# Kernel optimization log

Measured on AMD Instinct MI355X. Metric: run time of the kernel, lower is better.

Reference implementation:

```python
import jax, jax.numpy as jnp
import numpy as np

N_NODES = 50000
N_EDGES = 500000
IN_DIM = 256
HEADS = 4
OUT_C = 64
NEG_SLOPE = 0.2


def setup_inputs() -> dict:
    key = jax.random.key(0)
    ks = jax.random.split(key, 6)
    x = jax.random.normal(ks[0], (N_NODES, IN_DIM), dtype=jnp.float32)
    edge_index = jax.random.randint(ks[1], (2, N_EDGES), 0, N_NODES, dtype=jnp.int64)
    scale = 1.0 / np.sqrt(IN_DIM)
    W_l = jax.random.normal(ks[2], (IN_DIM, HEADS * OUT_C), dtype=jnp.float32) * scale
    W_r = jax.random.normal(ks[3], (IN_DIM, HEADS * OUT_C), dtype=jnp.float32) * scale
    b_l = jnp.zeros((HEADS * OUT_C,), dtype=jnp.float32)
    b_r = jnp.zeros((HEADS * OUT_C,), dtype=jnp.float32)
    att = jax.random.normal(ks[4], (HEADS, OUT_C), dtype=jnp.float32) * (1.0 / np.sqrt(OUT_C))
    bias = jnp.zeros((HEADS * OUT_C,), dtype=jnp.float32)
    return {"x": x, "edge_index": edge_index, "W_l": W_l, "b_l": b_l,
            "W_r": W_r, "b_r": b_r, "att": att, "bias": bias}


def _gatv2(x, edge_index, W_l, b_l, W_r, b_r, att, bias):
    N = x.shape[0]
    H, C = att.shape
    # add self loops (PyG GATv2Conv default add_self_loops=True)
    loop = jnp.arange(N, dtype=edge_index.dtype)
    src = jnp.concatenate([edge_index[0], loop])  # message sources (x_j)
    dst = jnp.concatenate([edge_index[1], loop])  # aggregation targets (x_i)
    x_l = (x @ W_l + b_l).reshape(N, H, C)  # source-side projection
    x_r = (x @ W_r + b_r).reshape(N, H, C)  # target-side projection
    # GATv2 attention logits: a^T LeakyReLU(x_l[src] + x_r[dst])
    e = jax.nn.leaky_relu(x_l[src] + x_r[dst], NEG_SLOPE)  # [E, H, C]
    logits = jnp.einsum('ehc,hc->eh', e, att)              # [E, H]
    # segmented softmax over incoming edges of each dst node
    m = jax.ops.segment_max(logits, dst, num_segments=N)   # [N, H]
    ex = jnp.exp(logits - m[dst])
    denom = jax.ops.segment_sum(ex, dst, num_segments=N)   # [N, H]
    alpha = ex / denom[dst]                                # [E, H]
    # weighted scatter-aggregation of source messages
    out = jax.ops.segment_sum(x_l[src] * alpha[:, :, None], dst, num_segments=N)  # [N, H, C]
    return out.reshape(N, H * C) + bias


def reference(x, edge_index, W_l, b_l, W_r, b_r, att, bias):
    out = _gatv2(x, edge_index, W_l, b_l, W_r, b_r, att, bias)  # [N, H*C]
    # wrapper: single relation -> reshape(-1, 1, output_dim) and cat on dim=1
    return out.reshape(-1, 1, HEADS * OUT_C)
```

## Files before the change

### kernel.cpp

```cpp
#include <hip/hip_runtime.h>
#include <hip/hip_bf16.h>
#include <math.h>

#define N_NODES 50000
#define N_PAD   50048
#define N_EDGES 500000
#define E_TOT   550000
#define HC      256
#define NHC     512
#define HEADS   4
#define NEG     0.2f

typedef __attribute__((ext_vector_type(8))) short short8;
typedef __attribute__((ext_vector_type(4))) float f32x4;
typedef __attribute__((ext_vector_type(2))) float f32x2;

__device__ __forceinline__ ushort f2bf(float f) {
    union { float f; unsigned u; } c; c.f = f;
    unsigned u = c.u;
    unsigned rounded = u + 0x7FFFu + ((u >> 16) & 1u);
    return (ushort)(rounded >> 16);
}

static constexpr size_t OFF_COUNTS = 0;
static constexpr size_t OFF_CUR    = OFF_COUNTS + (size_t)N_NODES * 4;
static constexpr size_t OFF_ROWS   = OFF_CUR + (size_t)N_NODES * 4;
static constexpr size_t OFF_SRCS   = OFF_ROWS + (size_t)(N_NODES + 1) * 4;
static constexpr size_t OFF_BSUM   = OFF_SRCS + (size_t)E_TOT * 4;
static constexpr size_t OFF_MODE   = OFF_BSUM + 64 * 4;
static constexpr size_t OFF_XB     = ((OFF_MODE + 4 + 255) / 256) * 256;
static constexpr size_t OFF_WT     = OFF_XB + (size_t)N_PAD * HC * 2;
static constexpr size_t OFF_XLB    = OFF_WT + (size_t)NHC * HC * 2;
static constexpr size_t OFF_XRB    = OFF_XLB + (size_t)N_NODES * HC * 2;

__device__ __forceinline__ int get_src(const int* __restrict__ ei, int mode, int e) {
    if (e >= N_EDGES) return e - N_EDGES;
    return mode ? ei[2 * e] : ei[e];
}
__device__ __forceinline__ int get_dst(const int* __restrict__ ei, int mode, int e) {
    if (e >= N_EDGES) return e - N_EDGES;
    return mode ? ei[2 * (N_EDGES + e)] : ei[N_EDGES + e];
}

#define XBLK 6256
#define WBLK 512
__global__ __launch_bounds__(256) void prep_kernel(
        const float* __restrict__ x, const float* __restrict__ Wl,
        const float* __restrict__ Wr, const int* __restrict__ ei,
        ushort* __restrict__ xb, ushort* __restrict__ wt, int* __restrict__ mode) {
    const int b = blockIdx.x;
    if (b < XBLK) {
        size_t i = ((size_t)b * 256 + threadIdx.x) * 8;
        if (i >= (size_t)N_PAD * HC) return;
        ushort o[8];
        if (i < (size_t)N_NODES * HC) {
            float4 v0 = *(const float4*)(x + i);
            float4 v1 = *(const float4*)(x + i + 4);
            o[0] = f2bf(v0.x); o[1] = f2bf(v0.y); o[2] = f2bf(v0.z); o[3] = f2bf(v0.w);
            o[4] = f2bf(v1.x); o[5] = f2bf(v1.y); o[6] = f2bf(v1.z); o[7] = f2bf(v1.w);
        } else {
#pragma unroll
            for (int j = 0; j < 8; ++j) o[j] = 0;
        }
        *(short8*)(xb + i) = *(short8*)o;
    } else if (b < XBLK + WBLK) {
        int i = (b - XBLK) * 256 + threadIdx.x;
        int n = i >> 8, k = i & 255;
        float v = (n < HC) ? Wl[(size_t)k * HC + n] : Wr[(size_t)k * HC + (n - HC)];
        wt[i] = f2bf(v);
    } else {
        __shared__ int any;
        if (threadIdx.x == 0) any = 0;
        __syncthreads();
        if (ei[2 * threadIdx.x + 1] != 0) atomicOr(&any, 1);
        __syncthreads();
        if (threadIdx.x == 0) mode[0] = (any == 0) ? 1 : 0;
    }
}

#define BM 128
#define BK 32
__global__ __launch_bounds__(256) void mfma_gemm_kernel(
        const __hip_bfloat16* __restrict__ xb, const __hip_bfloat16* __restrict__ wt,
        const float* __restrict__ bl, const float* __restrict__ br,
        ushort* __restrict__ xlb, ushort* __restrict__ xrb) {
    __shared__ __hip_bfloat16 As[2][BM * BK];
    __shared__ __hip_bfloat16 Bs[2][BM * BK];
    const int t    = threadIdx.x;
    const int lane = t & 63;
    const int wid  = t >> 6;
    const int wr   = wid >> 1, wc = wid & 1;
    const int brow = blockIdx.x * BM;
    const int bcol = blockIdx.y * BM;

    auto stage = [&](int buf, int k0) {
#pragma unroll
        for (int r = 0; r < 2; ++r) {
            int c = r * 256 + t;
            const __hip_bfloat16* ga = xb + ((size_t)(brow + (c >> 2)) * HC + k0 + (c & 3) * 8);
            __builtin_amdgcn_global_load_lds(
                (const __attribute__((address_space(1))) void*)ga,
                (__attribute__((address_space(3))) void*)((char*)&As[buf][0] + c * 16),
                16, 0, 0);
        }
#pragma unroll
        for (int r = 0; r < 2; ++r) {
            int c = r * 256 + t;
            const __hip_bfloat16* gb = wt + ((size_t)(bcol + (c >> 2)) * HC + k0 + (c & 3) * 8);
            __builtin_amdgcn_global_load_lds(
                (const __attribute__((address_space(1))) void*)gb,
                (__attribute__((address_space(3))) void*)((char*)&Bs[buf][0] + c * 16),
                16, 0, 0);
        }
    };

    f32x4 acc[4][4];
#pragma unroll
    for (int m = 0; m < 4; ++m)
#pragma unroll
        for (int n = 0; n < 4; ++n) acc[m][n] = (f32x4)0.f;

    stage(0, 0);
    __syncthreads();

    const int rsub = lane & 15;
    const int koff = (lane >> 4) * 16;

    for (int kk = 0; kk < 8; ++kk) {
        const int cur = kk & 1;
        if (kk < 7) stage(cur ^ 1, (kk + 1) * BK);
        short8 a[4], b[4];
#pragma unroll
        for (int m = 0; m < 4; ++m)
            a[m] = *(const short8*)((const char*)&As[cur][0] +
                    (wr * 64 + m * 16 + rsub) * (BK * 2) + koff);
#pragma unroll
        for (int n = 0; n < 4; ++n)
            b[n] = *(const short8*)((const char*)&Bs[cur][0] +
                    (wc * 64 + n * 16 + rsub) * (BK * 2) + koff);
#pragma unroll
        for (int m = 0; m < 4; ++m)
#pragma unroll
            for (int n = 0; n < 4; ++n)
                acc[m][n] = __builtin_amdgcn_mfma_f32_16x16x32_bf16(a[m], b[n], acc[m][n], 0, 0, 0);
        __syncthreads();
    }

    ushort* dst = (bcol < HC) ? xlb : xrb;
    const float* bvec = (bcol < HC) ? bl : br;
    const int cb = bcol & (HC - 1);
#pragma unroll
    for (int m = 0; m < 4; ++m) {
#pragma unroll
        for (int n = 0; n < 4; ++n) {
            int col = cb + wc * 64 + n * 16 + (lane & 15);
            float bv = bvec[col];
#pragma unroll
            for (int j = 0; j < 4; ++j) {
                int row = brow + wr * 64 + m * 16 + (lane >> 4) * 4 + j;
                if (row < N_NODES) dst[(size_t)row * HC + col] = f2bf(acc[m][n][j] + bv);
            }
        }
    }
}

__global__ void count_kernel(const int* __restrict__ ei, const int* __restrict__ mode,
                             int* __restrict__ counts) {
    int e = blockIdx.x * blockDim.x + threadIdx.x;
    if (e < E_TOT) atomicAdd(&counts[get_dst(ei, *mode, e)], 1);
}

__global__ void scan1_kernel(const int* __restrict__ counts, int* __restrict__ rows,
                             int* __restrict__ bsum) {
    __shared__ int sdata[256];
    const int t = threadIdx.x;
    const int base = blockIdx.x * 1024 + t * 4;
    int v[4]; int s = 0;
#pragma unroll
    for (int j = 0; j < 4; ++j) {
        int idx = base + j;
        v[j] = (idx < N_NODES) ? counts[idx] : 0;
        s += v[j];
    }
    sdata[t] = s;
    __syncthreads();
    for (int off = 1; off < 256; off <<= 1) {
        int xv = (t >= off) ? sdata[t - off] : 0;
        __syncthreads();
        sdata[t] += xv;
        __syncthreads();
    }
    int run = sdata[t] - s;
#pragma unroll
    for (int j = 0; j < 4; ++j) {
        int idx = base + j;
        if (idx < N_NODES) rows[idx] = run;
        run += v[j];
    }
    if (t == 255) bsum[blockIdx.x] = sdata[255];
}

__global__ void scan2_kernel(int* __restrict__ bsum, int* __restrict__ rows) {
    if (threadIdx.x == 0 && blockIdx.x == 0) {
        int run = 0;
        for (int b = 0; b < 49; ++b) { int xv = bsum[b]; bsum[b] = run; run += xv; }
        rows[N_NODES] = E_TOT;
    }
}

__global__ void scan3_kernel(int* __restrict__ rows, const int* __restrict__ bsum) {
    int idx = blockIdx.x * 256 + threadIdx.x;
    if (idx < N_NODES) rows[idx] += bsum[idx >> 10];
}

__global__ void fill_kernel(const int* __restrict__ ei, const int* __restrict__ mode,
                            const int* __restrict__ rows, int* __restrict__ cursor,
                            int* __restrict__ srcs) {
    int e = blockIdx.x * blockDim.x + threadIdx.x;
    if (e < E_TOT) {
        int md = *mode;
        int d = get_dst(ei, md, e);
        int s = get_src(ei, md, e);
        int pos = atomicAdd(&cursor[d], 1);
        srcs[rows[d] + pos] = s;
    }
}

__global__ __launch_bounds__(256) void fused_agg_kernel(
        const ushort* __restrict__ xlb, const ushort* __restrict__ xrb,
        const float* __restrict__ att,
        const int* __restrict__ rows, const int* __restrict__ srcs,
        const float* __restrict__ bias, float* __restrict__ out) {
    const int lane = threadIdx.x & 63;
    const int n = (blockIdx.x * 256 + threadIdx.x) >> 6;
    if (n >= N_NODES) return;
    const int half = lane >> 5;
    const int sl   = lane & 31;
    const int start = rows[n], end = rows[n + 1];

    f32x2 xr2[4], at2[4];
    {
        uint4 c = *(const uint4*)(xrb + (size_t)n * HC + sl * 8);
        unsigned w[4] = {c.x, c.y, c.z, c.w};
#pragma unroll
        for (int j = 0; j < 4; ++j) {
            xr2[j][0] = __uint_as_float(w[j] << 16);
            xr2[j][1] = __uint_as_float(w[j] & 0xffff0000u);
        }
        float4 a0 = *(const float4*)&att[sl * 8];
        float4 a1 = *(const float4*)&att[sl * 8 + 4];
        at2[0][0] = a0.x; at2[0][1] = a0.y; at2[1][0] = a0.z; at2[1][1] = a0.w;
        at2[2][0] = a1.x; at2[2][1] = a1.y; at2[3][0] = a1.z; at2[3][1] = a1.w;
    }

    f32x2 acc2[4];
#pragma unroll
    for (int j = 0; j < 4; ++j) acc2[j] = (f32x2)0.f;
    float sm = 0.f;

    int i = start + half;
    uint4 rA = make_uint4(0, 0, 0, 0);
    int sB = -1;
    if (i < end) rA = *(const uint4*)(xlb + (size_t)srcs[i] * HC + sl * 8);
    if (i + 2 < end) sB = srcs[i + 2];

    for (; i < end; i += 2) {
        uint4 r = rA;
        if (sB >= 0) rA = *(const uint4*)(xlb + (size_t)sB * HC + sl * 8);
        sB = (i + 4 < end) ? srcs[i + 4] : -1;

        unsigned w[4] = {r.x, r.y, r.z, r.w};
        f32x2 xv[4];
#pragma unroll
        for (int j = 0; j < 4; ++j) {
            xv[j][0] = __uint_as_float(w[j] << 16);
            xv[j][1] = __uint_as_float(w[j] & 0xffff0000u);
        }

        f32x2 p2 = (f32x2)0.f;
#pragma unroll
        for (int j = 0; j < 4; ++j) {
            f32x2 v = xv[j] + xr2[j];
            f32x2 lk = __builtin_elementwise_max(v, v * NEG);
            p2 = lk * at2[j] + p2;
        }
        float p = p2[0] + p2[1];
        p += __shfl_xor(p, 1, 64);
        p += __shfl_xor(p, 2, 64);
        p += __shfl_xor(p, 4, 64);

        float wgt = __expf(p);
        sm += wgt;
        f32x2 w2; w2[0] = wgt; w2[1] = wgt;
#pragma unroll
        for (int j = 0; j < 4; ++j) acc2[j] = xv[j] * w2 + acc2[j];
    }

    sm += __shfl_xor(sm, 32, 64);
#pragma unroll
    for (int j = 0; j < 4; ++j) {
        acc2[j][0] += __shfl_xor(acc2[j][0], 32, 64);
        acc2[j][1] += __shfl_xor(acc2[j][1], 32, 64);
    }

    if (half == 0) {
        const float inv = 1.0f / sm;
        float4 b0 = *(const float4*)&bias[sl * 8];
        float4 b1 = *(const float4*)&bias[sl * 8 + 4];
        float4 o0, o1;
        o0.x = fmaf(acc2[0][0], inv, b0.x); o0.y = fmaf(acc2[0][1], inv, b0.y);
        o0.z = fmaf(acc2[1][0], inv, b0.z); o0.w = fmaf(acc2[1][1], inv, b0.w);
        o1.x = fmaf(acc2[2][0], inv, b1.x); o1.y = fmaf(acc2[2][1], inv, b1.y);
        o1.z = fmaf(acc2[3][0], inv, b1.z); o1.w = fmaf(acc2[3][1], inv, b1.w);
        *(float4*)&out[(size_t)n * HC + sl * 8]     = o0;
        *(float4*)&out[(size_t)n * HC + sl * 8 + 4] = o1;
    }
}

extern "C" void kernel_launch(void* const* d_in, const int* in_sizes, int n_in,
                              void* d_out, int out_size, void* d_ws, size_t ws_size,
                              hipStream_t stream) {
    const float* x    = (const float*)d_in[0];
    const int*   ei   = (const int*)d_in[1];
    const float* Wl   = (const float*)d_in[2];
    const float* bl   = (const float*)d_in[3];
    const float* Wr   = (const float*)d_in[4];
    const float* br   = (const float*)d_in[5];
    const float* att  = (const float*)d_in[6];
    const float* bias = (const float*)d_in[7];
    float* out = (float*)d_out;

    char* ws = (char*)d_ws;
    int*   counts = (int*)(ws + OFF_COUNTS);
    int*   cursor = (int*)(ws + OFF_CUR);
    int*   rows   = (int*)(ws + OFF_ROWS);
    int*   srcs   = (int*)(ws + OFF_SRCS);
    int*   bsum   = (int*)(ws + OFF_BSUM);
    int*   mode   = (int*)(ws + OFF_MODE);
    ushort* xb    = (ushort*)(ws + OFF_XB);
    ushort* wt    = (ushort*)(ws + OFF_WT);
    ushort* xlb   = (ushort*)(ws + OFF_XLB);
    ushort* xrb   = (ushort*)(ws + OFF_XRB);

    (void)hipMemsetAsync(counts, 0, (size_t)N_NODES * 8, stream);

    prep_kernel<<<XBLK + WBLK + 1, 256, 0, stream>>>(x, Wl, Wr, ei, xb, wt, mode);

    dim3 ggrid(N_PAD / BM, NHC / BM);
    mfma_gemm_kernel<<<ggrid, 256, 0, stream>>>(
        (const __hip_bfloat16*)xb, (const __hip_bfloat16*)wt, bl, br, xlb, xrb);

    count_kernel<<<(E_TOT + 255) / 256, 256, 0, stream>>>(ei, mode, counts);
    scan1_kernel<<<49, 256, 0, stream>>>(counts, rows, bsum);
    scan2_kernel<<<1, 64, 0, stream>>>(bsum, rows);
    scan3_kernel<<<(N_NODES + 255) / 256, 256, 0, stream>>>(rows, bsum);
    fill_kernel<<<(E_TOT + 255) / 256, 256, 0, stream>>>(ei, mode, rows, cursor, srcs);

    fused_agg_kernel<<<(N_NODES + 3) / 4, 256, 0, stream>>>(
        xlb, xrb, att, rows, srcs, bias, out);
}
```

Before: 169.6 us.

## Stage GEMM epilogue through swizzled LDS, widen agg lanes, fold memset into prep

Three changes land together. The GEMM epilogue now writes bf16 results into a swizzled shared-memory tile and copies whole rows out as 16-byte stores, replacing scattered 2-byte global stores. The aggregation kernel processes four edges per wavefront, with each lane covering 16 channels, which halves the shuffle reduction depth per edge and doubles the per-lane load width. Zeroing of the counts/cursor buffer moves into extra blocks of the prep kernel, removing a separate memset launch at the cost of higher register use in the aggregation kernel.

```diff
diff --git a/kernel.cpp b/kernel.cpp
--- a/kernel.cpp
+++ b/kernel.cpp
@@ -44,10 +44,12 @@
 
 #define XBLK 6256
 #define WBLK 512
+#define ZBLK 98
 __global__ __launch_bounds__(256) void prep_kernel(
         const float* __restrict__ x, const float* __restrict__ Wl,
         const float* __restrict__ Wr, const int* __restrict__ ei,
-        ushort* __restrict__ xb, ushort* __restrict__ wt, int* __restrict__ mode) {
+        ushort* __restrict__ xb, ushort* __restrict__ wt,
+        int* __restrict__ cz, int* __restrict__ mode) {
     const int b = blockIdx.x;
     if (b < XBLK) {
         size_t i = ((size_t)b * 256 + threadIdx.x) * 8;
@@ -68,6 +70,9 @@
         int n = i >> 8, k = i & 255;
         float v = (n < HC) ? Wl[(size_t)k * HC + n] : Wr[(size_t)k * HC + (n - HC)];
         wt[i] = f2bf(v);
+    } else if (b < XBLK + WBLK + ZBLK) {
+        int i4 = (b - XBLK - WBLK) * 256 + threadIdx.x;
+        if (i4 < 2 * N_NODES / 4) *(int4*)(cz + i4 * 4) = make_int4(0, 0, 0, 0);
     } else {
         __shared__ int any;
         if (threadIdx.x == 0) any = 0;
@@ -84,8 +89,9 @@
         const __hip_bfloat16* __restrict__ xb, const __hip_bfloat16* __restrict__ wt,
         const float* __restrict__ bl, const float* __restrict__ br,
         ushort* __restrict__ xlb, ushort* __restrict__ xrb) {
-    __shared__ __hip_bfloat16 As[2][BM * BK];
-    __shared__ __hip_bfloat16 Bs[2][BM * BK];
+    __shared__ ushort smem[4 * BM * BK];
+    auto AS = [&](int buf) { return (__hip_bfloat16*)(smem + buf * BM * BK); };
+    auto BS = [&](int buf) { return (__hip_bfloat16*)(smem + 2 * BM * BK + buf * BM * BK); };
     const int t    = threadIdx.x;
     const int lane = t & 63;
     const int wid  = t >> 6;
@@ -100,7 +106,7 @@
             const __hip_bfloat16* ga = xb + ((size_t)(brow + (c >> 2)) * HC + k0 + (c & 3) * 8);
             __builtin_amdgcn_global_load_lds(
                 (const __attribute__((address_space(1))) void*)ga,
-                (__attribute__((address_space(3))) void*)((char*)&As[buf][0] + c * 16),
+                (__attribute__((address_space(3))) void*)((char*)AS(buf) + c * 16),
                 16, 0, 0);
         }
 #pragma unroll
@@ -109,7 +115,7 @@
             const __hip_bfloat16* gb = wt + ((size_t)(bcol + (c >> 2)) * HC + k0 + (c & 3) * 8);
             __builtin_amdgcn_global_load_lds(
                 (const __attribute__((address_space(1))) void*)gb,
-                (__attribute__((address_space(3))) void*)((char*)&Bs[buf][0] + c * 16),
+                (__attribute__((address_space(3))) void*)((char*)BS(buf) + c * 16),
                 16, 0, 0);
         }
     };
@@ -132,11 +138,11 @@
         short8 a[4], b[4];
 #pragma unroll
         for (int m = 0; m < 4; ++m)
-            a[m] = *(const short8*)((const char*)&As[cur][0] +
+            a[m] = *(const short8*)((const char*)AS(cur) +
                     (wr * 64 + m * 16 + rsub) * (BK * 2) + koff);
 #pragma unroll
         for (int n = 0; n < 4; ++n)
-            b[n] = *(const short8*)((const char*)&Bs[cur][0] +
+            b[n] = *(const short8*)((const char*)BS(cur) +
                     (wc * 64 + n * 16 + rsub) * (BK * 2) + koff);
 #pragma unroll
         for (int m = 0; m < 4; ++m)
@@ -153,12 +159,26 @@
     for (int m = 0; m < 4; ++m) {
 #pragma unroll
         for (int n = 0; n < 4; ++n) {
-            int col = cb + wc * 64 + n * 16 + (lane & 15);
-            float bv = bvec[col];
+            int c_loc = wc * 64 + n * 16 + (lane & 15);
+            float bv = bvec[cb + c_loc];
 #pragma unroll
             for (int j = 0; j < 4; ++j) {
-                int row = brow + wr * 64 + m * 16 + (lane >> 4) * 4 + j;
-                if (row < N_NODES) dst[(size_t)row * HC + col] = f2bf(acc[m][n][j] + bv);
+                int r_loc = wr * 64 + m * 16 + (lane >> 4) * 4 + j;
+                smem[r_loc * 128 + (((c_loc >> 3) ^ (r_loc & 15)) * 8) + (c_loc & 7)] =
+                    f2bf(acc[m][n][j] + bv);
+            }
+        }
+    }
+    __syncthreads();
+    {
+        const int r = t >> 1, hf = t & 1;
+        if (brow + r < N_NODES) {
+            ushort* gout = dst + (size_t)(brow + r) * HC + cb + hf * 64;
+#pragma unroll
+            for (int i = 0; i < 8; ++i) {
+                int ci = hf * 8 + i;
+                uint4 v = *(const uint4*)&smem[r * 128 + ((ci ^ (r & 15)) * 8)];
+                *(uint4*)(gout + i * 8) = v;
             }
         }
     }
@@ -234,52 +254,66 @@
     const int lane = threadIdx.x & 63;
     const int n = (blockIdx.x * 256 + threadIdx.x) >> 6;
     if (n >= N_NODES) return;
-    const int half = lane >> 5;
-    const int sl   = lane & 31;
+    const int eslot = lane >> 4;
+    const int chunk = lane & 15;
+    const int cbase = chunk * 16;
     const int start = rows[n], end = rows[n + 1];
 
-    f32x2 xr2[4], at2[4];
+    f32x2 xr2[8], at2[8];
     {
-        uint4 c = *(const uint4*)(xrb + (size_t)n * HC + sl * 8);
-        unsigned w[4] = {c.x, c.y, c.z, c.w};
-#pragma unroll
-        for (int j = 0; j < 4; ++j) {
-            xr2[j][0] = __uint_as_float(w[j] << 16);
-            xr2[j][1] = __uint_as_float(w[j] & 0xffff0000u);
-        }
-        float4 a0 = *(const float4*)&att[sl * 8];
-        float4 a1 = *(const float4*)&att[sl * 8 + 4];
+        uint4 c0 = *(const uint4*)(xrb + (size_t)n * HC + cbase);
+        uint4 c1 = *(const uint4*)(xrb + (size_t)n * HC + cbase + 8);
+        unsigned w0[8] = {c0.x, c0.y, c0.z, c0.w, c1.x, c1.y, c1.z, c1.w};
+#pragma unroll
+        for (int j = 0; j < 8; ++j) {
+            xr2[j][0] = __uint_as_float(w0[j] << 16);
+            xr2[j][1] = __uint_as_float(w0[j] & 0xffff0000u);
+        }
+        float4 a0 = *(const float4*)&att[cbase];
+        float4 a1 = *(const float4*)&att[cbase + 4];
+        float4 a2 = *(const float4*)&att[cbase + 8];
+        float4 a3 = *(const float4*)&att[cbase + 12];
         at2[0][0] = a0.x; at2[0][1] = a0.y; at2[1][0] = a0.z; at2[1][1] = a0.w;
         at2[2][0] = a1.x; at2[2][1] = a1.y; at2[3][0] = a1.z; at2[3][1] = a1.w;
-    }
-
-    f32x2 acc2[4];
-#pragma unroll
-    for (int j = 0; j < 4; ++j) acc2[j] = (f32x2)0.f;
+        at2[4][0] = a2.x; at2[4][1] = a2.y; at2[5][0] = a2.z; at2[5][1] = a2.w;
+        at2[6][0] = a3.x; at2[6][1] = a3.y; at2[7][0] = a3.z; at2[7][1] = a3.w;
+    }
+
+    f32x2 acc2[8];
+#pragma unroll
+    for (int j = 0; j < 8; ++j) acc2[j] = (f32x2)0.f;
     float sm = 0.f;
 
-    int i = start + half;
-    uint4 rA = make_uint4(0, 0, 0, 0);
+    int i = start + eslot;
+    uint4 rA0 = make_uint4(0, 0, 0, 0), rA1 = make_uint4(0, 0, 0, 0);
     int sB = -1;
-    if (i < end) rA = *(const uint4*)(xlb + (size_t)srcs[i] * HC + sl * 8);
-    if (i + 2 < end) sB = srcs[i + 2];
-
-    for (; i < end; i += 2) {
-        uint4 r = rA;
-        if (sB >= 0) rA = *(const uint4*)(xlb + (size_t)sB * HC + sl * 8);
-        sB = (i + 4 < end) ? srcs[i + 4] : -1;
-
-        unsigned w[4] = {r.x, r.y, r.z, r.w};
-        f32x2 xv[4];
-#pragma unroll
-        for (int j = 0; j < 4; ++j) {
+    if (i < end) {
+        const ushort* p = xlb + (size_t)srcs[i] * HC + cbase;
+        rA0 = *(const uint4*)p;
+        rA1 = *(const uint4*)(p + 8);
+    }
+    if (i + 4 < end) sB = srcs[i + 4];
+
+    for (; i < end; i += 4) {
+        uint4 r0 = rA0, r1 = rA1;
+        if (sB >= 0) {
+            const ushort* p = xlb + (size_t)sB * HC + cbase;
+            rA0 = *(const uint4*)p;
+            rA1 = *(const uint4*)(p + 8);
+        }
+        sB = (i + 8 < end) ? srcs[i + 8] : -1;
+
+        unsigned w[8] = {r0.x, r0.y, r0.z, r0.w, r1.x, r1.y, r1.z, r1.w};
+        f32x2 xv[8];
+#pragma unroll
+        for (int j = 0; j < 8; ++j) {
             xv[j][0] = __uint_as_float(w[j] << 16);
             xv[j][1] = __uint_as_float(w[j] & 0xffff0000u);
         }
 
         f32x2 p2 = (f32x2)0.f;
 #pragma unroll
-        for (int j = 0; j < 4; ++j) {
+        for (int j = 0; j < 8; ++j) {
             f32x2 v = xv[j] + xr2[j];
             f32x2 lk = __builtin_elementwise_max(v, v * NEG);
             p2 = lk * at2[j] + p2;
@@ -287,33 +321,37 @@
         float p = p2[0] + p2[1];
         p += __shfl_xor(p, 1, 64);
         p += __shfl_xor(p, 2, 64);
-        p += __shfl_xor(p, 4, 64);
 
         float wgt = __expf(p);
         sm += wgt;
         f32x2 w2; w2[0] = wgt; w2[1] = wgt;
 #pragma unroll
-        for (int j = 0; j < 4; ++j) acc2[j] = xv[j] * w2 + acc2[j];
-    }
-
+        for (int j = 0; j < 8; ++j) acc2[j] = xv[j] * w2 + acc2[j];
+    }
+
+    sm += __shfl_xor(sm, 16, 64);
     sm += __shfl_xor(sm, 32, 64);
 #pragma unroll
-    for (int j = 0; j < 4; ++j) {
+    for (int j = 0; j < 8; ++j) {
+        acc2[j][0] += __shfl_xor(acc2[j][0], 16, 64);
+        acc2[j][1] += __shfl_xor(acc2[j][1], 16, 64);
         acc2[j][0] += __shfl_xor(acc2[j][0], 32, 64);
         acc2[j][1] += __shfl_xor(acc2[j][1], 32, 64);
     }
 
-    if (half == 0) {
+    if (eslot == 0) {
         const float inv = 1.0f / sm;
-        float4 b0 = *(const float4*)&bias[sl * 8];
-        float4 b1 = *(const float4*)&bias[sl * 8 + 4];
-        float4 o0, o1;
-        o0.x = fmaf(acc2[0][0], inv, b0.x); o0.y = fmaf(acc2[0][1], inv, b0.y);
-        o0.z = fmaf(acc2[1][0], inv, b0.z); o0.w = fmaf(acc2[1][1], inv, b0.w);
-        o1.x = fmaf(acc2[2][0], inv, b1.x); o1.y = fmaf(acc2[2][1], inv, b1.y);
-        o1.z = fmaf(acc2[3][0], inv, b1.z); o1.w = fmaf(acc2[3][1], inv, b1.w);
-        *(float4*)&out[(size_t)n * HC + sl * 8]     = o0;
-        *(float4*)&out[(size_t)n * HC + sl * 8 + 4] = o1;
+        float* o = out + (size_t)n * HC + cbase;
+#pragma unroll
+        for (int q = 0; q < 4; ++q) {
+            float4 bv = *(const float4*)&bias[cbase + q * 4];
+            float4 ov;
+            ov.x = fmaf(acc2[2 * q][0],     inv, bv.x);
+            ov.y = fmaf(acc2[2 * q][1],     inv, bv.y);
+            ov.z = fmaf(acc2[2 * q + 1][0], inv, bv.z);
+            ov.w = fmaf(acc2[2 * q + 1][1], inv, bv.w);
+            *(float4*)(o + q * 4) = ov;
+        }
     }
 }
 
@@ -342,9 +380,8 @@
     ushort* xlb   = (ushort*)(ws + OFF_XLB);
     ushort* xrb   = (ushort*)(ws + OFF_XRB);
 
-    (void)hipMemsetAsync(counts, 0, (size_t)N_NODES * 8, stream);
-
-    prep_kernel<<<XBLK + WBLK + 1, 256, 0, stream>>>(x, Wl, Wr, ei, xb, wt, mode);
+    prep_kernel<<<XBLK + WBLK + ZBLK + 1, 256, 0, stream>>>(
+        x, Wl, Wr, ei, xb, wt, counts, mode);
 
     dim3 ggrid(N_PAD / BM, NHC / BM);
     mfma_gemm_kernel<<<ggrid, 256, 0, stream>>>(
```

Measured after the change: 169.3 us. Within noise of the previous version (-0.1%).
